# Kernel tuning notes

Measured on AMD Instinct MI355X. Metric: run time of the kernel, lower is better.

The kernel has to match this reference:

```python
import jax, jax.numpy as jnp
import numpy as np

EPS = 1e-5

@jax.custom_vjp
def round_ste(x):
    return jnp.round(x)

def _round_fwd(x):
    return jnp.round(x), None

def _round_bwd(_, g):
    return (g,)

round_ste.defvjp(_round_fwd, _round_bwd)


def setup_inputs() -> dict:
    key = jax.random.key(0)
    ks = jax.random.split(key, 4)
    x = jax.random.normal(ks[0], (16, 64, 128, 128), dtype=jnp.float32)
    # small init so conv outputs stay in a sane range
    W = jax.random.normal(ks[1], (128, 64, 3, 3), dtype=jnp.float32) * 0.05
    gamma = jnp.ones((128,), dtype=jnp.float32)
    beta = jnp.zeros((128,), dtype=jnp.float32)
    mean = jax.random.normal(ks[2], (128,), dtype=jnp.float32) * 0.1
    var = jax.random.uniform(ks[3], (128,), dtype=jnp.float32) * 0.5 + 0.5
    # Brevitas QuantReLU default learned max ~6.0 (relu6-like init)
    act_scale = jnp.ones((1,), dtype=jnp.float32) * 6.0
    return {"x": x, "W": W, "gamma": gamma, "beta": beta,
            "mean": mean, "var": var, "act_scale": act_scale}


def reference(x, W, gamma, beta, mean, var, act_scale):
    # --- Int8 per-tensor weight quant-dequant (symmetric, scale = maxabs/127) ---
    w_scale = jnp.max(jnp.abs(W)) / 127.0
    qW = jnp.clip(round_ste(W / w_scale), -127.0, 127.0) * w_scale
    # --- conv2d, stride 1, padding 1, no bias (NCHW / OIHW) ---
    y = jax.lax.conv_general_dilated(
        x, qW, window_strides=(1, 1), padding=[(1, 1), (1, 1)],
        dimension_numbers=("NCHW", "OIHW", "NCHW"))
    # --- BatchNorm (inference form with running stats) ---
    scale = (gamma / jnp.sqrt(var + EPS))[None, :, None, None]
    shift = (beta - gamma * mean / jnp.sqrt(var + EPS))[None, :, None, None]
    y = y * scale + shift
    # --- QuantReLU: relu + uint8 per-tensor quant-dequant ---
    y = jax.nn.relu(y)
    s = act_scale[0] / 255.0
    return jnp.clip(round_ste(y / s), 0.0, 255.0) * s
```

## Files before the change

### kernel.cpp

```cpp
#include <hip/hip_runtime.h>
#include <math.h>

typedef __bf16 bf16x8 __attribute__((ext_vector_type(8)));
typedef float  f32x16 __attribute__((ext_vector_type(16)));

#define CIN    64
#define KOUT   128
#define HGT    128
#define WID    128
#define NBATCH 16
#define BN_EPS 1e-5f

#define WQ_OFF   256u
#define XT_OFF   (1u << 20)
#define WS_NEED  ((size_t)XT_OFF + (size_t)NBATCH * HGT * WID * CIN * 2)

__global__ __launch_bounds__(256) void wmax_kernel(const float* __restrict__ W,
                                                   unsigned* __restrict__ wsmax) {
    int idx = blockIdx.x * 256 + threadIdx.x;
    const float4* W4 = (const float4*)W;
    float4 v = W4[idx];
    float m = fmaxf(fmaxf(fabsf(v.x), fabsf(v.y)), fmaxf(fabsf(v.z), fabsf(v.w)));
    #pragma unroll
    for (int off = 32; off > 0; off >>= 1)
        m = fmaxf(m, __shfl_xor(m, off));
    __shared__ float red[4];
    if ((threadIdx.x & 63) == 0) red[threadIdx.x >> 6] = m;
    __syncthreads();
    if (threadIdx.x == 0) {
        m = fmaxf(fmaxf(red[0], red[1]), fmaxf(red[2], red[3]));
        atomicMax(wsmax, __float_as_uint(m));
    }
}

__global__ __launch_bounds__(256) void pack_w(const float* __restrict__ W,
                                              const unsigned* __restrict__ wsmax,
                                              __bf16* __restrict__ wqp) {
    int bid = blockIdx.x;
    int tap = bid % 9, cs = bid / 9;
    int t = threadIdx.x;
    int lane = t & 63, mf = t >> 6;
    float ws = __uint_as_float(*wsmax) / 127.0f;
    int kout  = mf * 32 + (lane & 31);
    int cbase = cs * 16 + (lane >> 5) * 8;
    bf16x8 o;
    #pragma unroll
    for (int j = 0; j < 8; ++j) {
        float w = W[(size_t)(kout * 64 + cbase + j) * 9 + tap];
        float q = rintf(w / ws);
        q = fminf(fmaxf(q, -127.f), 127.f);
        o[j] = (__bf16)q;
    }
    *(bf16x8*)(wqp + (((size_t)bid * 4 + mf) * 64 + lane) * 8) = o;
}

__global__ __launch_bounds__(256) void xform(const float* __restrict__ x,
                                             __bf16* __restrict__ xT) {
    __shared__ float t[CIN * 32];
    int bid = blockIdx.x;
    int wt = bid & 3;
    int h  = (bid >> 2) & 127;
    int n  = bid >> 9;
    int w0 = wt * 32;
    int tid = threadIdx.x;
    const float* src = x + ((size_t)n * CIN * HGT + h) * WID + w0;
    int wlane = tid & 31;
    int cbase = tid >> 5;
    #pragma unroll
    for (int it = 0; it < 8; ++it) {
        int c = cbase + it * 8;
        t[c * 32 + (wlane ^ (c & 31))] = src[(size_t)c * HGT * WID + wlane];
    }
    __syncthreads();
    int w = tid >> 3;
    int chunk = tid & 7;
    bf16x8 o;
    #pragma unroll
    for (int j = 0; j < 8; ++j) {
        int c = chunk * 8 + j;
        o[j] = (__bf16)t[c * 32 + (w ^ (c & 31))];
    }
    *(bf16x8*)(xT + (((size_t)n * HGT + h) * WID + w0 + w) * CIN + chunk * 8) = o;
}

__global__ __launch_bounds__(256, 2) void conv_mfma(
    const __bf16* __restrict__ xT, const __bf16* __restrict__ wqp,
    const float* __restrict__ gamma, const float* __restrict__ beta,
    const float* __restrict__ mean, const float* __restrict__ var,
    const float* __restrict__ act_scale, const unsigned* __restrict__ wsmax,
    float* __restrict__ out)
{
    __shared__ uint4 xs[2592];
    __shared__ float sc2[KOUT], sh2[KOUT];

    const int bid = blockIdx.x;
    const int wb = bid & 7, hb = (bid >> 3) & 7, n = bid >> 6;
    const int h0 = hb * 16, w0 = wb * 16;
    const int tid  = threadIdx.x;
    const int lane = tid & 63;
    const int wave = tid >> 6;
    const int wm = wave & 1;
    const int wn = wave >> 1;

    const float s_act = act_scale[0] / 255.0f;
    if (tid < KOUT) {
        float ws  = __uint_as_float(*wsmax) / 127.0f;
        float isd = 1.0f / sqrtf(var[tid] + BN_EPS);
        float sc  = ws * gamma[tid] * isd;
        float sh  = beta[tid] - gamma[tid] * mean[tid] * isd;
        sc2[tid] = sc / s_act;
        sh2[tid] = sh / s_act;
    }

    const __bf16* xn = xT + (size_t)n * HGT * WID * CIN;
    for (int it = tid; it < 2592; it += 256) {
        int pl = it >> 3, chunk = it & 7;
        int r = pl / 18, cc = pl - r * 18;
        int gh = h0 - 1 + r, gw = w0 - 1 + cc;
        uint4 v = make_uint4(0u, 0u, 0u, 0u);
        if ((unsigned)gh < HGT && (unsigned)gw < WID)
            v = *(const uint4*)(xn + ((size_t)gh * WID + gw) * CIN + chunk * 8);
        xs[pl * 8 + (chunk ^ (pl & 7))] = v;
    }
    __syncthreads();

    const int wl = lane & 15;
    const int rl = (lane >> 4) & 1;
    const int kh = lane >> 5;

    f32x16 acc[2][4];
    #pragma unroll
    for (int a = 0; a < 2; ++a)
        #pragma unroll
        for (int b = 0; b < 4; ++b)
            #pragma unroll
            for (int r = 0; r < 16; ++r) acc[a][b][r] = 0.0f;

    #pragma unroll
    for (int cs = 0; cs < 4; ++cs) {
        bf16x8 a[2][9];
        #pragma unroll
        for (int tap = 0; tap < 9; ++tap) {
            const __bf16* wp = wqp + ((((size_t)cs * 9 + tap) * 4 + wm * 2) * 64 + lane) * 8;
            a[0][tap] = *(const bf16x8*)(wp);
            a[1][tap] = *(const bf16x8*)(wp + 64 * 8);
        }
        const int chb = cs * 2 + kh;
        #pragma unroll
        for (int tap = 0; tap < 9; ++tap) {
            const int dy = tap / 3, dx = tap - dy * 3;
            #pragma unroll
            for (int nf = 0; nf < 4; ++nf) {
                const int pl = (wn * 8 + nf * 2 + rl + dy) * 18 + wl + dx;
                bf16x8 b = *(const bf16x8*)&xs[pl * 8 + (chb ^ (pl & 7))];
                acc[0][nf] = __builtin_amdgcn_mfma_f32_32x32x16_bf16(a[0][tap], b, acc[0][nf], 0, 0, 0);
                acc[1][nf] = __builtin_amdgcn_mfma_f32_32x32x16_bf16(a[1][tap], b, acc[1][nf], 0, 0, 0);
            }
        }
    }

    const int wpix = w0 + wl;
    #pragma unroll
    for (int mf = 0; mf < 2; ++mf) {
        #pragma unroll
        for (int nf = 0; nf < 4; ++nf) {
            const int hpix = h0 + wn * 8 + nf * 2 + rl;
            #pragma unroll
            for (int reg = 0; reg < 16; ++reg) {
                int k = wm * 64 + mf * 32 + 4 * kh + (reg & 3) + 8 * (reg >> 2);
                float t = fmaf(acc[mf][nf][reg], sc2[k], sh2[k]);
                t = fmaxf(t, 0.0f);
                float q = fminf(rintf(t), 255.0f);
                out[(((size_t)n * KOUT + k) * HGT + hpix) * WID + wpix] = q * s_act;
            }
        }
    }
}

#define CB 4
#define TH 8
#define KB 8
__global__ __launch_bounds__(256) void conv_fallback(
    const float* __restrict__ x, const float* __restrict__ W,
    const float* __restrict__ gamma, const float* __restrict__ beta,
    const float* __restrict__ mean, const float* __restrict__ var,
    const float* __restrict__ act_scale, const unsigned* __restrict__ wsmax,
    float* __restrict__ out)
{
    __shared__ float xsf[CB][TH + 2][WID + 2];
    __shared__ float wsh[CB][9][KB];
    const int bid = blockIdx.x;
    const int hg = bid & 15, kg = (bid >> 4) & 15, n = bid >> 8;
    const int h0 = hg * TH, k0 = kg * KB;
    const int tid = threadIdx.x;
    const int tx = tid & 31, ty = tid >> 5;
    float acc[4][KB];
    #pragma unroll
    for (int j = 0; j < 4; ++j)
        #pragma unroll
        for (int kk = 0; kk < KB; ++kk) acc[j][kk] = 0.f;
    const float w_scale = __uint_as_float(*wsmax) / 127.0f;
    const float* xn = x + (size_t)n * CIN * HGT * WID;
    for (int c0 = 0; c0 < CIN; c0 += CB) {
        __syncthreads();
        for (int i = tid; i < CB * (TH + 2) * (WID + 2); i += 256) {
            int cc = i / ((TH + 2) * (WID + 2));
            int r  = i - cc * ((TH + 2) * (WID + 2));
            int yy = r / (WID + 2);
            int xx = r - yy * (WID + 2);
            int gh = h0 - 1 + yy, gw = xx - 1;
            float v = 0.f;
            if ((unsigned)gh < HGT && (unsigned)gw < WID)
                v = xn[(size_t)(c0 + cc) * HGT * WID + gh * WID + gw];
            xsf[cc][yy][xx] = v;
        }
        for (int i = tid; i < CB * 9 * KB; i += 256) {
            int cc = i / (9 * KB);
            int r  = i - cc * (9 * KB);
            int tap = r / KB, kk = r - tap * KB;
            float w = W[(size_t)((k0 + kk) * CIN + (c0 + cc)) * 9 + tap];
            float q = rintf(w / w_scale);
            q = fminf(fmaxf(q, -127.f), 127.f);
            wsh[cc][tap][kk] = q * w_scale;
        }
        __syncthreads();
        #pragma unroll
        for (int cc = 0; cc < CB; ++cc)
            #pragma unroll
            for (int dy = 0; dy < 3; ++dy) {
                float w0a[KB], w1a[KB], w2a[KB];
                #pragma unroll
                for (int kk = 0; kk < KB; ++kk) {
                    w0a[kk] = wsh[cc][dy * 3 + 0][kk];
                    w1a[kk] = wsh[cc][dy * 3 + 1][kk];
                    w2a[kk] = wsh[cc][dy * 3 + 2][kk];
                }
                const float* row = &xsf[cc][ty + dy][0];
                #pragma unroll
                for (int j = 0; j < 4; ++j) {
                    float v0 = row[tx + 32 * j + 0];
                    float v1 = row[tx + 32 * j + 1];
                    float v2 = row[tx + 32 * j + 2];
                    #pragma unroll
                    for (int kk = 0; kk < KB; ++kk) {
                        acc[j][kk] = fmaf(v0, w0a[kk], acc[j][kk]);
                        acc[j][kk] = fmaf(v1, w1a[kk], acc[j][kk]);
                        acc[j][kk] = fmaf(v2, w2a[kk], acc[j][kk]);
                    }
                }
            }
    }
    const float s_act = act_scale[0] / 255.0f;
    const float inv_s = 1.0f / s_act;
    const int h = h0 + ty;
    #pragma unroll
    for (int kk = 0; kk < KB; ++kk) {
        int k = k0 + kk;
        float isd = 1.0f / sqrtf(var[k] + BN_EPS);
        float sc = gamma[k] * isd;
        float sh = beta[k] - gamma[k] * mean[k] * isd;
        float* orow = out + (((size_t)n * KOUT + k) * HGT + h) * WID;
        #pragma unroll
        for (int j = 0; j < 4; ++j) {
            float y = fmaf(acc[j][kk], sc, sh);
            y = fmaxf(y, 0.f);
            float q = rintf(y * inv_s);
            q = fminf(q, 255.f);
            orow[tx + 32 * j] = q * s_act;
        }
    }
}

extern "C" void kernel_launch(void* const* d_in, const int* in_sizes, int n_in,
                              void* d_out, int out_size, void* d_ws, size_t ws_size,
                              hipStream_t stream) {
    const float* x         = (const float*)d_in[0];
    const float* W         = (const float*)d_in[1];
    const float* gamma     = (const float*)d_in[2];
    const float* beta      = (const float*)d_in[3];
    const float* mean      = (const float*)d_in[4];
    const float* var       = (const float*)d_in[5];
    const float* act_scale = (const float*)d_in[6];
    unsigned* wsmax = (unsigned*)d_ws;

    hipMemsetAsync(d_ws, 0, sizeof(unsigned), stream);
    wmax_kernel<<<72, 256, 0, stream>>>(W, wsmax);

    if (ws_size >= WS_NEED) {
        __bf16* wqp = (__bf16*)((char*)d_ws + WQ_OFF);
        __bf16* xT  = (__bf16*)((char*)d_ws + XT_OFF);
        pack_w<<<36, 256, 0, stream>>>(W, wsmax, wqp);
        xform<<<NBATCH * HGT * 4, 256, 0, stream>>>(x, xT);
        conv_mfma<<<NBATCH * 64, 256, 0, stream>>>(
            xT, wqp, gamma, beta, mean, var, act_scale, wsmax, (float*)d_out);
    } else {
        conv_fallback<<<4096, 256, 0, stream>>>(
            x, W, gamma, beta, mean, var, act_scale, wsmax, (float*)d_out);
    }
}
```

Before: 86.49 us.

## Retile conv block to 8x32 pixels and reuse LDS input fragments across rows

Changes the block tile from 16x16 to 8 rows by 32 columns so each MFMA N-fragment covers one full 32-pixel row. Each wave now loads a 6x3 set of input fragments from shared memory once per channel slice and reuses them across the three kernel rows and four output rows, replacing 36 separate LDS reads per slice with 18. Weight fragments are loaded per kernel row instead of all nine taps up front. The aim is to cut LDS traffic and give wider contiguous output stores, at the cost of a slightly larger halo and more live registers.

Measured after the change: 84.40 us. -2.4%, faster.

```diff
diff --git a/kernel.cpp b/kernel.cpp
--- a/kernel.cpp
+++ b/kernel.cpp
@@ -90,17 +90,17 @@
     const float* __restrict__ act_scale, const unsigned* __restrict__ wsmax,
     float* __restrict__ out)
 {
-    __shared__ uint4 xs[2592];
+    __shared__ uint4 xs[2720];
     __shared__ float sc2[KOUT], sh2[KOUT];
 
     const int bid = blockIdx.x;
-    const int wb = bid & 7, hb = (bid >> 3) & 7, n = bid >> 6;
-    const int h0 = hb * 16, w0 = wb * 16;
+    const int wb = bid & 3, hb = (bid >> 2) & 15, n = bid >> 6;
+    const int h0 = hb * 8, w0 = wb * 32;
     const int tid  = threadIdx.x;
     const int lane = tid & 63;
     const int wave = tid >> 6;
     const int wm = wave & 1;
-    const int wn = wave >> 1;
+    const int wr = wave >> 1;
 
     const float s_act = act_scale[0] / 255.0f;
     if (tid < KOUT) {
@@ -113,9 +113,9 @@
     }
 
     const __bf16* xn = xT + (size_t)n * HGT * WID * CIN;
-    for (int it = tid; it < 2592; it += 256) {
+    for (int it = tid; it < 2720; it += 256) {
         int pl = it >> 3, chunk = it & 7;
-        int r = pl / 18, cc = pl - r * 18;
+        int r = pl / 34, cc = pl - r * 34;
         int gh = h0 - 1 + r, gw = w0 - 1 + cc;
         uint4 v = make_uint4(0u, 0u, 0u, 0u);
         if ((unsigned)gh < HGT && (unsigned)gw < WID)
@@ -124,8 +124,7 @@
     }
     __syncthreads();
 
-    const int wl = lane & 15;
-    const int rl = (lane >> 4) & 1;
+    const int nn = lane & 31;
     const int kh = lane >> 5;
 
     f32x16 acc[2][4];
@@ -138,33 +137,42 @@
 
     #pragma unroll
     for (int cs = 0; cs < 4; ++cs) {
-        bf16x8 a[2][9];
-        #pragma unroll
-        for (int tap = 0; tap < 9; ++tap) {
-            const __bf16* wp = wqp + ((((size_t)cs * 9 + tap) * 4 + wm * 2) * 64 + lane) * 8;
-            a[0][tap] = *(const bf16x8*)(wp);
-            a[1][tap] = *(const bf16x8*)(wp + 64 * 8);
-        }
         const int chb = cs * 2 + kh;
-        #pragma unroll
-        for (int tap = 0; tap < 9; ++tap) {
-            const int dy = tap / 3, dx = tap - dy * 3;
+        bf16x8 B[6][3];
+        #pragma unroll
+        for (int rr = 0; rr < 6; ++rr) {
+            #pragma unroll
+            for (int dx = 0; dx < 3; ++dx) {
+                const int pl = (wr * 4 + rr) * 34 + nn + dx;
+                B[rr][dx] = *(const bf16x8*)&xs[pl * 8 + (chb ^ (pl & 7))];
+            }
+        }
+        #pragma unroll
+        for (int dy = 0; dy < 3; ++dy) {
+            bf16x8 A[2][3];
+            #pragma unroll
+            for (int dx = 0; dx < 3; ++dx) {
+                const __bf16* wp = wqp + ((((size_t)cs * 9 + dy * 3 + dx) * 4 + wm * 2) * 64 + lane) * 8;
+                A[0][dx] = *(const bf16x8*)(wp);
+                A[1][dx] = *(const bf16x8*)(wp + 64 * 8);
+            }
             #pragma unroll
             for (int nf = 0; nf < 4; ++nf) {
-                const int pl = (wn * 8 + nf * 2 + rl + dy) * 18 + wl + dx;
-                bf16x8 b = *(const bf16x8*)&xs[pl * 8 + (chb ^ (pl & 7))];
-                acc[0][nf] = __builtin_amdgcn_mfma_f32_32x32x16_bf16(a[0][tap], b, acc[0][nf], 0, 0, 0);
-                acc[1][nf] = __builtin_amdgcn_mfma_f32_32x32x16_bf16(a[1][tap], b, acc[1][nf], 0, 0, 0);
-            }
-        }
-    }
-
-    const int wpix = w0 + wl;
+                #pragma unroll
+                for (int dx = 0; dx < 3; ++dx) {
+                    acc[0][nf] = __builtin_amdgcn_mfma_f32_32x32x16_bf16(A[0][dx], B[nf + dy][dx], acc[0][nf], 0, 0, 0);
+                    acc[1][nf] = __builtin_amdgcn_mfma_f32_32x32x16_bf16(A[1][dx], B[nf + dy][dx], acc[1][nf], 0, 0, 0);
+                }
+            }
+        }
+    }
+
+    const int wpix = w0 + nn;
     #pragma unroll
     for (int mf = 0; mf < 2; ++mf) {
         #pragma unroll
         for (int nf = 0; nf < 4; ++nf) {
-            const int hpix = h0 + wn * 8 + nf * 2 + rl;
+            const int hpix = h0 + wr * 4 + nf;
             #pragma unroll
             for (int reg = 0; reg < 16; ++reg) {
                 int k = wm * 64 + mf * 32 + 4 * kh + (reg & 3) + 8 * (reg >> 2);
```
